# Performance work log

Measured on AMD Instinct MI355X. Metric: run time of the kernel, lower is better.

## Reference

```python
import jax, jax.numpy as jnp
import numpy as np

B, N, D = 4, 4096, 128

def setup_inputs() -> dict:
    key = jax.random.key(0)
    k1, k2 = jax.random.split(key)
    x = jax.random.normal(k1, (B, N, D), dtype=jnp.float32)
    a = jax.random.normal(k2, (2 * D, 1), dtype=jnp.float32)
    return {"x": x, "a": a}

def reference(x, a):
    # matmul(cat([x_i, x_j], -1), a) == x_i @ a1 + x_j @ a2, so avoid the
    # O(B*N*N*2D) concat: compute two O(B*N) projections and broadcast-add.
    a1 = a[:D, 0]   # [D]
    a2 = a[D:, 0]   # [D]
    s_i = x @ a1    # [B, N]  (row / source term)
    s_j = x @ a2    # [B, N]  (col / target term)
    e = s_i[:, :, None] + s_j[:, None, :]          # [B, N, N]
    e = jnp.where(e > 0, e, 0.2 * e)               # leaky_relu(0.2)
    attention = jax.nn.softmax(e, axis=-1)         # row softmax
    return attention[..., None]                    # [B, N, N, 1]
```

## Files before the change

kernel.cpp:

```cpp
#include <hip/hip_runtime.h>

#define BB 4
#define NN 4096
#define DD 128

__global__ __launch_bounds__(256) void score_kernel(const float* __restrict__ x,
                                                    const float* __restrict__ a,
                                                    float* __restrict__ si,
                                                    float* __restrict__ sj) {
    int wave = threadIdx.x >> 6;
    int lane = threadIdx.x & 63;
    int row  = blockIdx.x * 4 + wave;
    const float* xr = x + (size_t)row * DD;
    float x0 = xr[lane];
    float x1 = xr[lane + 64];
    float d1 = x0 * a[lane]      + x1 * a[lane + 64];
    float d2 = x0 * a[DD + lane] + x1 * a[DD + lane + 64];
    #pragma unroll
    for (int off = 32; off > 0; off >>= 1) {
        d1 += __shfl_down(d1, off, 64);
        d2 += __shfl_down(d2, off, 64);
    }
    if (lane == 0) {
        si[row] = d1;
        sj[row] = d2;
    }
}

__global__ __launch_bounds__(256) void softmax_kernel(const float* __restrict__ si_g,
                                                      const float* __restrict__ sj_g,
                                                      float* __restrict__ out) {
    __shared__ float sj[NN];
    __shared__ float red[4];

    const int b   = blockIdx.x >> 12;
    const int i   = blockIdx.x & (NN - 1);
    const int tid = threadIdx.x;

    const float* sjb = sj_g + b * NN;
    float lmax = -INFINITY;
    #pragma unroll
    for (int k = 0; k < NN / 256; ++k) {
        float v = sjb[tid + k * 256];
        sj[tid + k * 256] = v;
        lmax = fmaxf(lmax, v);
    }
    #pragma unroll
    for (int off = 32; off > 0; off >>= 1)
        lmax = fmaxf(lmax, __shfl_down(lmax, off, 64));
    if ((tid & 63) == 0) red[tid >> 6] = lmax;
    __syncthreads();
    const float sjmax = fmaxf(fmaxf(red[0], red[1]), fmaxf(red[2], red[3]));

    const float sival = si_g[b * NN + i];
    float m = sival + sjmax;
    m = m > 0.f ? m : 0.2f * m;

    float p[16];
    float lsum = 0.f;
    #pragma unroll
    for (int g = 0; g < 4; ++g) {
        const int j0 = g * 1024 + tid * 4;
        #pragma unroll
        for (int k = 0; k < 4; ++k) {
            float e = sival + sj[j0 + k];
            e = e > 0.f ? e : 0.2f * e;
            float pv = __expf(e - m);
            p[g * 4 + k] = pv;
            lsum += pv;
        }
    }
    #pragma unroll
    for (int off = 32; off > 0; off >>= 1)
        lsum += __shfl_down(lsum, off, 64);
    __syncthreads();
    if ((tid & 63) == 0) red[tid >> 6] = lsum;
    __syncthreads();
    const float inv = 1.f / (red[0] + red[1] + red[2] + red[3]);

    float* orow = out + (size_t)(b * NN + i) * NN;
    #pragma unroll
    for (int g = 0; g < 4; ++g) {
        const int j0 = g * 1024 + tid * 4;
        float4 v = make_float4(p[g * 4 + 0] * inv, p[g * 4 + 1] * inv,
                               p[g * 4 + 2] * inv, p[g * 4 + 3] * inv);
        *reinterpret_cast<float4*>(orow + j0) = v;
    }
}

extern "C" void kernel_launch(void* const* d_in, const int* in_sizes, int n_in,
                              void* d_out, int out_size, void* d_ws, size_t ws_size,
                              hipStream_t stream) {
    const float* x = (const float*)d_in[0];
    const float* a = (const float*)d_in[1];
    float* out = (float*)d_out;
    float* si = (float*)d_ws;
    float* sj = si + BB * NN;

    score_kernel<<<(BB * NN) / 4, 256, 0, stream>>>(x, a, si, sj);
    softmax_kernel<<<BB * NN, 256, 0, stream>>>(si, sj, out);
}
```

Before: 54.15 us.

## Process multiple rows per block with wave-per-row softmax and register-held sj

```diff
diff --git a/kernel.cpp b/kernel.cpp
--- a/kernel.cpp
+++ b/kernel.cpp
@@ -3,6 +3,7 @@
 #define BB 4
 #define NN 4096
 #define DD 128
+#define RB 8
 
 __global__ __launch_bounds__(256) void score_kernel(const float* __restrict__ x,
                                                     const float* __restrict__ a,
@@ -30,61 +31,61 @@
 __global__ __launch_bounds__(256) void softmax_kernel(const float* __restrict__ si_g,
                                                       const float* __restrict__ sj_g,
                                                       float* __restrict__ out) {
-    __shared__ float sj[NN];
     __shared__ float red[4];
 
-    const int b   = blockIdx.x >> 12;
-    const int i   = blockIdx.x & (NN - 1);
-    const int tid = threadIdx.x;
+    const int bpb  = NN / RB;
+    const int b    = blockIdx.x / bpb;
+    const int i0   = (blockIdx.x % bpb) * RB;
+    const int wave = threadIdx.x >> 6;
+    const int lane = threadIdx.x & 63;
 
     const float* sjb = sj_g + b * NN;
+    float4 sjv[16];
     float lmax = -INFINITY;
     #pragma unroll
-    for (int k = 0; k < NN / 256; ++k) {
-        float v = sjb[tid + k * 256];
-        sj[tid + k * 256] = v;
-        lmax = fmaxf(lmax, v);
+    for (int g = 0; g < 16; ++g) {
+        sjv[g] = *reinterpret_cast<const float4*>(sjb + g * 256 + lane * 4);
+        lmax = fmaxf(fmaxf(fmaxf(sjv[g].x, sjv[g].y), fmaxf(sjv[g].z, sjv[g].w)), lmax);
     }
     #pragma unroll
-    for (int off = 32; off > 0; off >>= 1)
-        lmax = fmaxf(lmax, __shfl_down(lmax, off, 64));
-    if ((tid & 63) == 0) red[tid >> 6] = lmax;
+    for (int off = 1; off < 64; off <<= 1)
+        lmax = fmaxf(lmax, __shfl_xor(lmax, off, 64));
+    if (lane == 0) red[wave] = lmax;
     __syncthreads();
     const float sjmax = fmaxf(fmaxf(red[0], red[1]), fmaxf(red[2], red[3]));
 
-    const float sival = si_g[b * NN + i];
-    float m = sival + sjmax;
-    m = m > 0.f ? m : 0.2f * m;
+    #pragma unroll
+    for (int r = 0; r < RB / 4; ++r) {
+        const int i = i0 + wave * (RB / 4) + r;
+        const float sival = si_g[b * NN + i];
+        float m = sival + sjmax;
+        m = m > 0.f ? m : 0.2f * m;
 
-    float p[16];
-    float lsum = 0.f;
-    #pragma unroll
-    for (int g = 0; g < 4; ++g) {
-        const int j0 = g * 1024 + tid * 4;
+        float lsum = 0.f;
         #pragma unroll
-        for (int k = 0; k < 4; ++k) {
-            float e = sival + sj[j0 + k];
-            e = e > 0.f ? e : 0.2f * e;
-            float pv = __expf(e - m);
-            p[g * 4 + k] = pv;
-            lsum += pv;
+        for (int g = 0; g < 16; ++g) {
+            float e0 = sival + sjv[g].x; e0 = (e0 > 0.f ? e0 : 0.2f * e0) - m;
+            float e1 = sival + sjv[g].y; e1 = (e1 > 0.f ? e1 : 0.2f * e1) - m;
+            float e2 = sival + sjv[g].z; e2 = (e2 > 0.f ? e2 : 0.2f * e2) - m;
+            float e3 = sival + sjv[g].w; e3 = (e3 > 0.f ? e3 : 0.2f * e3) - m;
+            lsum += __expf(e0) + __expf(e1) + __expf(e2) + __expf(e3);
         }
-    }
-    #pragma unroll
-    for (int off = 32; off > 0; off >>= 1)
-        lsum += __shfl_down(lsum, off, 64);
-    __syncthreads();
-    if ((tid & 63) == 0) red[tid >> 6] = lsum;
-    __syncthreads();
-    const float inv = 1.f / (red[0] + red[1] + red[2] + red[3]);
+        #pragma unroll
+        for (int off = 1; off < 64; off <<= 1)
+            lsum += __shfl_xor(lsum, off, 64);
+        const float inv = 1.f / lsum;
 
-    float* orow = out + (size_t)(b * NN + i) * NN;
-    #pragma unroll
-    for (int g = 0; g < 4; ++g) {
-        const int j0 = g * 1024 + tid * 4;
-        float4 v = make_float4(p[g * 4 + 0] * inv, p[g * 4 + 1] * inv,
-                               p[g * 4 + 2] * inv, p[g * 4 + 3] * inv);
-        *reinterpret_cast<float4*>(orow + j0) = v;
+        float* orow = out + (size_t)(b * NN + i) * NN;
+        #pragma unroll
+        for (int g = 0; g < 16; ++g) {
+            float e0 = sival + sjv[g].x; e0 = (e0 > 0.f ? e0 : 0.2f * e0) - m;
+            float e1 = sival + sjv[g].y; e1 = (e1 > 0.f ? e1 : 0.2f * e1) - m;
+            float e2 = sival + sjv[g].z; e2 = (e2 > 0.f ? e2 : 0.2f * e2) - m;
+            float e3 = sival + sjv[g].w; e3 = (e3 > 0.f ? e3 : 0.2f * e3) - m;
+            float4 v = make_float4(__expf(e0) * inv, __expf(e1) * inv,
+                                   __expf(e2) * inv, __expf(e3) * inv);
+            *reinterpret_cast<float4*>(orow + g * 256 + lane * 4) = v;
+        }
     }
 }
 
@@ -98,5 +99,5 @@
     float* sj = si + BB * NN;
 
     score_kernel<<<(BB * NN) / 4, 256, 0, stream>>>(x, a, si, sj);
-    softmax_kernel<<<BB * NN, 256, 0, stream>>>(si, sj, out);
+    softmax_kernel<<<(BB * NN) / RB, 256, 0, stream>>>(si, sj, out);
 }
```

New measurement: 52.62 us. 1.03x faster.
